# Kernel optimization log

Hardware: AMD Instinct MI355X
Metric: run time of the kernel (lower is better)

Reference implementation:

```python
import jax, jax.numpy as jnp
import numpy as np

N_NODES = 100000
N_EDGES = 800000
D = 64   # embedding_size
H = 4    # heads


def setup_inputs() -> dict:
    key = jax.random.key(0)
    k1, k2, k3, k4, k5 = jax.random.split(key, 5)
    xavier = float(np.sqrt(2.0 / (D + D)))  # xavier_uniform scale (approx, via normal)
    all_embeddings = jax.random.normal(k1, (N_NODES, D), dtype=jnp.float32)
    Wq = jax.random.normal(k2, (D, D), dtype=jnp.float32) * xavier
    Wk = jax.random.normal(k3, (D, D), dtype=jnp.float32) * xavier
    Wv = jax.random.normal(k4, (D, D), dtype=jnp.float32) * xavier
    edge_index = jax.random.randint(k5, (2, N_EDGES), 0, N_NODES, dtype=jnp.int32)
    return {"all_embeddings": all_embeddings, "Wq": Wq, "Wk": Wk, "Wv": Wv,
            "edge_index": edge_index}


def reference(all_embeddings, Wq, Wk, Wv, edge_index):
    rows, cols = edge_index[0], edge_index[1]
    n_nodes = all_embeddings.shape[0]
    e = rows.shape[0]
    dh = D // H

    row_emb = all_embeddings[rows]           # [E, D] gather
    col_emb = all_embeddings[cols]           # [E, D] gather

    q = (row_emb @ Wq).reshape(e, H, dh)     # [E, H, dh]
    k = (col_emb @ Wk).reshape(e, H, dh)
    v = (col_emb @ Wv).reshape(e, H, dh)

    att = jnp.einsum('ehd,ehd->eh', q, k)    # per-edge, per-head score
    att = jnp.clip(att, -10.0, 10.0)
    exp_att = jnp.exp(att)                   # [E, H]

    # segment softmax denominator over edges sharing the same destination row
    att_norm = jax.ops.segment_sum(exp_att, rows, num_segments=n_nodes)  # [N, H]
    att = exp_att / (att_norm[rows] + 1e-8)  # [E, H]

    out_e = (att[:, :, None] * v).reshape(e, D)  # [E, D] weighted values
    out = jax.ops.segment_sum(out_e, rows, num_segments=n_nodes)  # [N, D] scatter-add
    return out
```

## Files before the change

kernel.cpp:

```cpp
#include <hip/hip_runtime.h>
#include <math.h>

constexpr int D = 64;
constexpr int H = 4;
constexpr int EB = 8192;


typedef __attribute__((ext_vector_type(8))) short bf16x8;
typedef __attribute__((ext_vector_type(4))) float f32x4;

__device__ __forceinline__ unsigned short f32_to_bf16(float f) {
    const unsigned int u = __float_as_uint(f);
    return (unsigned short)((u + 0x7FFFu + ((u >> 16) & 1u)) >> 16);
}
__device__ __forceinline__ float bf16_to_f32(unsigned short h) {
    return __uint_as_float(((unsigned int)h) << 16);
}
__device__ __forceinline__ float bf16lo_f32(unsigned int w) {
    return __uint_as_float(w << 16);
}
__device__ __forceinline__ float bf16hi_f32(unsigned int w) {
    return __uint_as_float(w & 0xFFFF0000u);
}

__global__ __launch_bounds__(256) void prep_w_kernel(
    const float* __restrict__ Wq, const float* __restrict__ Wk,
    const float* __restrict__ Wv,
    unsigned short* __restrict__ WfH, unsigned short* __restrict__ WfL) {
    const float* W[3] = {Wq, Wk, Wv};
    for (int idx = blockIdx.x * 256 + threadIdx.x; idx < 3 * 4 * 2 * 64 * 8;
         idx += gridDim.x * 256) {
        const int j  = idx & 7;
        const int l  = (idx >> 3) & 63;
        const int ks = (idx >> 9) & 1;
        const int ct = (idx >> 10) & 3;
        const int mt = idx >> 12;
        const int krow = ks * 32 + (l >> 4) * 8 + j;
        const int col  = 4 * (l & 15) + ct;
        const float w  = W[mt][krow * 64 + col];
        const unsigned short h = f32_to_bf16(w);
        WfH[idx] = h;
        WfL[idx] = f32_to_bf16(w - bf16_to_f32(h));
    }
}

__global__ __launch_bounds__(256) void fused_qkv_hist_kernel(
    const float* __restrict__ emb,
    const unsigned short* __restrict__ WfH,
    const unsigned short* __restrict__ WfL,
    int N, float* __restrict__ Q, unsigned int* __restrict__ KVP,
    const int* __restrict__ rows, int* __restrict__ hist2d,
    int E, int NB, int HB) {
    __shared__ unsigned short sH[12288];
    __shared__ unsigned short sL[12288];
    __shared__ int h[512];
    const int tid = threadIdx.x;

    if ((int)blockIdx.x < HB) {
        const int blk = blockIdx.x;
        for (int b = tid; b < NB; b += 256) h[b] = 0;
        __syncthreads();
        const int e0 = blk * EB;
        const int e1 = min(E, e0 + EB);
        for (int i = e0 + tid; i < e1; i += 256)
            atomicAdd(&h[rows[i] >> 8], 1);
        __syncthreads();
        for (int b = tid; b < NB; b += 256) hist2d[blk * NB + b] = h[b];
        return;
    }

    const int bx = blockIdx.x - HB;
    {
        const uint4* gh = (const uint4*)WfH;
        const uint4* gl = (const uint4*)WfL;
        uint4* shh = (uint4*)sH;
        uint4* sll = (uint4*)sL;
        for (int k = tid; k < 1536; k += 256) {
            shh[k] = gh[k];
            sll[k] = gl[k];
        }
    }
    __syncthreads();

    const int wv = tid >> 6;
    const int l  = tid & 63;
    const int qd = l >> 4;
    const int m  = l & 15;

    for (int tile = 0; tile < 4; ++tile) {
        const int n0 = bx * 256 + tile * 64 + wv * 16;
        if (n0 >= N) break;

        bf16x8 aH[2], aL[2];
        {
            int node = n0 + m;
            if (node >= N) node = N - 1;
            const float4* ep = (const float4*)(emb + (size_t)node * 64);
#pragma unroll
            for (int ks = 0; ks < 2; ++ks) {
                const float4 a0 = ep[ks * 8 + qd * 2 + 0];
                const float4 a1 = ep[ks * 8 + qd * 2 + 1];
                const float f[8] = {a0.x, a0.y, a0.z, a0.w,
                                    a1.x, a1.y, a1.z, a1.w};
                bf16x8 fh, fl;
#pragma unroll
                for (int j = 0; j < 8; ++j) {
                    const unsigned short hh = f32_to_bf16(f[j]);
                    fh[j] = (short)hh;
                    fl[j] = (short)f32_to_bf16(f[j] - bf16_to_f32(hh));
                }
                aH[ks] = fh;
                aL[ks] = fl;
            }
        }

        f32x4 acc[3][4];
#pragma unroll
        for (int mt = 0; mt < 3; ++mt)
#pragma unroll
            for (int ct = 0; ct < 4; ++ct)
                acc[mt][ct] = (f32x4){0.f, 0.f, 0.f, 0.f};

#pragma unroll
        for (int mt = 0; mt < 3; ++mt) {
#pragma unroll
            for (int ct = 0; ct < 4; ++ct) {
#pragma unroll
                for (int ks = 0; ks < 2; ++ks) {
                    const int fi = (((mt * 4 + ct) * 2 + ks) * 64 + l) * 8;
                    bf16x8 bh = *(const bf16x8*)&sH[fi];
                    bf16x8 bl = *(const bf16x8*)&sL[fi];
                    acc[mt][ct] = __builtin_amdgcn_mfma_f32_16x16x32_bf16(
                        aH[ks], bh, acc[mt][ct], 0, 0, 0);
                    acc[mt][ct] = __builtin_amdgcn_mfma_f32_16x16x32_bf16(
                        aH[ks], bl, acc[mt][ct], 0, 0, 0);
                    acc[mt][ct] = __builtin_amdgcn_mfma_f32_16x16x32_bf16(
                        aL[ks], bh, acc[mt][ct], 0, 0, 0);
                }
            }
        }

#pragma unroll
        for (int r = 0; r < 4; ++r) {
            const int node = n0 + qd * 4 + r;
            if (node < N) {
                float4 oq;
                oq.x = acc[0][0][r]; oq.y = acc[0][1][r];
                oq.z = acc[0][2][r]; oq.w = acc[0][3][r];
                *(float4*)(Q + (size_t)node * 64 + 4 * m) = oq;

                uint4 kv;
                kv.x = (unsigned int)f32_to_bf16(acc[1][0][r]) |
                       ((unsigned int)f32_to_bf16(acc[1][1][r]) << 16);
                kv.y = (unsigned int)f32_to_bf16(acc[2][0][r]) |
                       ((unsigned int)f32_to_bf16(acc[2][1][r]) << 16);
                kv.z = (unsigned int)f32_to_bf16(acc[1][2][r]) |
                       ((unsigned int)f32_to_bf16(acc[1][3][r]) << 16);
                kv.w = (unsigned int)f32_to_bf16(acc[2][2][r]) |
                       ((unsigned int)f32_to_bf16(acc[2][3][r]) << 16);
                *(uint4*)(KVP + (size_t)node * 64 + 4 * m) = kv;
            }
        }
    }
}

__global__ __launch_bounds__(256) void scan2d_kernel(
    const int* __restrict__ hist2d, int* __restrict__ base2d,
    int* __restrict__ btot, int NBLK, int NB) {
    __shared__ int s[256];
    const int b   = blockIdx.x;
    const int tid = threadIdx.x;
    const int x = (tid < NBLK) ? hist2d[tid * NB + b] : 0;
    s[tid] = x;
    __syncthreads();
    for (int o = 1; o < 256; o <<= 1) {
        int v = 0;
        if (tid >= o) v = s[tid - o];
        __syncthreads();
        if (tid >= o) s[tid] += v;
        __syncthreads();
    }
    if (tid < NBLK) base2d[tid * NB + b] = s[tid] - x;
    if (tid == 255) btot[b] = s[255];
}

__global__ __launch_bounds__(256) void bscan_kernel(
    const int* __restrict__ btot, int* __restrict__ bbase, int NB) {
    __shared__ int s[256];
    __shared__ int carry;
    const int tid = threadIdx.x;
    if (tid == 0) carry = 0;
    __syncthreads();
    for (int base = 0; base < NB; base += 256) {
        const int i = base + tid;
        const int x = (i < NB) ? btot[i] : 0;
        s[tid] = x;
        __syncthreads();
        for (int o = 1; o < 256; o <<= 1) {
            int v = 0;
            if (tid >= o) v = s[tid - o];
            __syncthreads();
            if (tid >= o) s[tid] += v;
            __syncthreads();
        }
        if (i < NB) bbase[i] = carry + s[tid] - x;
        __syncthreads();
        if (tid == 255) carry += s[255];
        __syncthreads();
    }
}

__global__ __launch_bounds__(256) void scatter2d_kernel(
    const int* __restrict__ rows, const int* __restrict__ cols,
    const int* __restrict__ base2d, const int* __restrict__ bbase,
    unsigned int* __restrict__ tmp, int E, int NB) {
    __shared__ int lcur[512];
    const int tid = threadIdx.x;
    const int blk = blockIdx.x;
    for (int b = tid; b < NB; b += 256)
        lcur[b] = bbase[b] + base2d[blk * NB + b];
    __syncthreads();
    const int e0 = blk * EB;
    const int e1 = min(E, e0 + EB);
    for (int i = e0 + tid; i < e1; i += 256) {
        const int r = rows[i];
        const int c = cols[i];
        const int p = atomicAdd(&lcur[r >> 8], 1);
        tmp[p] = ((unsigned int)(r & 255) << 24) | (unsigned int)c;
    }
}

__global__ __launch_bounds__(256) void bucket_sort_kernel(
    const unsigned int* __restrict__ tmp, const int* __restrict__ bbase,
    const int* __restrict__ btot, int* __restrict__ off,
    int* __restrict__ sc, int N, int E, int NB) {
    __shared__ unsigned int ebuf[4096];
    __shared__ int sbuf[4096];
    __shared__ int lhist[256];
    __shared__ int s[256];
    __shared__ int lcur[256];
    const int b     = blockIdx.x;
    const int tid   = threadIdx.x;
    const int n0    = b * 256;
    const int gbase = bbase[b];
    const int cnt_b = btot[b];

    lhist[tid] = 0;
    __syncthreads();

    if (cnt_b <= 4096) {
        for (int i = tid; i < cnt_b; i += 256) {
            const unsigned int w = tmp[gbase + i];
            ebuf[i] = w;
            atomicAdd(&lhist[w >> 24], 1);
        }
        __syncthreads();
        const int x = lhist[tid];
        s[tid] = x;
        __syncthreads();
        for (int o = 1; o < 256; o <<= 1) {
            int v = 0;
            if (tid >= o) v = s[tid - o];
            __syncthreads();
            if (tid >= o) s[tid] += v;
            __syncthreads();
        }
        const int excl = s[tid] - x;
        const int node = n0 + tid;
        if (node < N) off[node] = gbase + excl;
        if (b == NB - 1 && tid == 0) off[N] = E;
        lcur[tid] = excl;
        __syncthreads();
        for (int i = tid; i < cnt_b; i += 256) {
            const unsigned int w = ebuf[i];
            const int p = atomicAdd(&lcur[w >> 24], 1);
            sbuf[p] = (int)(w & 0x00FFFFFFu);
        }
        __syncthreads();
        for (int i = tid; i < cnt_b; i += 256) sc[gbase + i] = sbuf[i];
    } else {
        for (int i = tid; i < cnt_b; i += 256)
            atomicAdd(&lhist[tmp[gbase + i] >> 24], 1);
        __syncthreads();
        const int x = lhist[tid];
        s[tid] = x;
        __syncthreads();
        for (int o = 1; o < 256; o <<= 1) {
            int v = 0;
            if (tid >= o) v = s[tid - o];
            __syncthreads();
            if (tid >= o) s[tid] += v;
            __syncthreads();
        }
        const int excl = s[tid] - x;
        const int node = n0 + tid;
        if (node < N) off[node] = gbase + excl;
        if (b == NB - 1 && tid == 0) off[N] = E;
        lcur[tid] = excl;
        __syncthreads();
        for (int i = tid; i < cnt_b; i += 256) {
            const unsigned int w = tmp[gbase + i];
            const int p = atomicAdd(&lcur[w >> 24], 1);
            sc[gbase + p] = (int)(w & 0x00FFFFFFu);
        }
    }
}

__device__ __forceinline__ void agg_step(const uint4 kv, const float4 q4,
                                         bool ok, float& aN, float& a0,
                                         float& a1, float& a2, float& a3) {
    float pp = q4.x * bf16lo_f32(kv.x);
    pp = fmaf(q4.y, bf16hi_f32(kv.x), pp);
    pp = fmaf(q4.z, bf16lo_f32(kv.z), pp);
    pp = fmaf(q4.w, bf16hi_f32(kv.z), pp);
    pp += __shfl_xor(pp, 1);
    pp += __shfl_xor(pp, 2);
    float e = __expf(fminf(fmaxf(pp, -10.f), 10.f));
    e = ok ? e : 0.f;
    aN += e;
    a0 = fmaf(e, bf16lo_f32(kv.y), a0);
    a1 = fmaf(e, bf16hi_f32(kv.y), a1);
    a2 = fmaf(e, bf16lo_f32(kv.w), a2);
    a3 = fmaf(e, bf16hi_f32(kv.w), a3);
}

__global__ __launch_bounds__(256) void aggregate_kernel(
    const int* __restrict__ off, const int* __restrict__ sc,
    const float* __restrict__ Q, const unsigned int* __restrict__ KVP,
    float* __restrict__ out, int N) {
    const int t = blockIdx.x * 256 + threadIdx.x;
    const int n = t >> 6;
    const int l = t & 63;
    if (n >= N) return;
    const int d  = l & 15;
    const int es = l >> 4;

    const int off0 = off[n];
    const int off1 = off[n + 1];
    const int deg  = off1 - off0;
    const float4 q4 = *(const float4*)(Q + (size_t)n * 64 + 4 * d);

    float aN = 0.f, a0 = 0.f, a1 = 0.f, a2 = 0.f, a3 = 0.f;

    for (int base = 0; base < deg; base += 64) {
        const int cnt = min(64, deg - base);
        int myc = 0;
        if (l < cnt) myc = sc[off0 + base + l];
        const int nst = (cnt + 3) >> 2;
        int si = 0;
        for (; si + 4 <= nst; si += 4) {
            const int e0 = si * 4 + es;
            const bool ok3 = e0 + 12 < cnt;
            const int c0 = __shfl(myc, e0);
            const int c1 = __shfl(myc, e0 + 4);
            const int c2 = __shfl(myc, e0 + 8);
            const int c3 = __shfl(myc, ok3 ? e0 + 12 : 0);
            const uint4 kv0 = *(const uint4*)(KVP + (size_t)c0 * 64 + 4 * d);
            const uint4 kv1 = *(const uint4*)(KVP + (size_t)c1 * 64 + 4 * d);
            const uint4 kv2 = *(const uint4*)(KVP + (size_t)c2 * 64 + 4 * d);
            const uint4 kv3 = *(const uint4*)(KVP + (size_t)c3 * 64 + 4 * d);
            agg_step(kv0, q4, true, aN, a0, a1, a2, a3);
            agg_step(kv1, q4, true, aN, a0, a1, a2, a3);
            agg_step(kv2, q4, true, aN, a0, a1, a2, a3);
            agg_step(kv3, q4, ok3, aN, a0, a1, a2, a3);
        }
        if (si + 2 <= nst) {
            const int e0 = si * 4 + es;
            const bool ok1 = e0 + 4 < cnt;
            const int c0 = __shfl(myc, e0);
            const int c1 = __shfl(myc, ok1 ? e0 + 4 : 0);
            const uint4 kv0 = *(const uint4*)(KVP + (size_t)c0 * 64 + 4 * d);
            const uint4 kv1 = *(const uint4*)(KVP + (size_t)c1 * 64 + 4 * d);
            agg_step(kv0, q4, true, aN, a0, a1, a2, a3);
            agg_step(kv1, q4, ok1, aN, a0, a1, a2, a3);
            si += 2;
        }
        if (si < nst) {
            const int e0 = si * 4 + es;
            const bool ok0 = e0 < cnt;
            const int c0 = __shfl(myc, ok0 ? e0 : 0);
            const uint4 kv0 = *(const uint4*)(KVP + (size_t)c0 * 64 + 4 * d);
            agg_step(kv0, q4, ok0, aN, a0, a1, a2, a3);
        }
    }

    aN += __shfl_xor(aN, 16);  aN += __shfl_xor(aN, 32);
    a0 += __shfl_xor(a0, 16);  a0 += __shfl_xor(a0, 32);
    a1 += __shfl_xor(a1, 16);  a1 += __shfl_xor(a1, 32);
    a2 += __shfl_xor(a2, 16);  a2 += __shfl_xor(a2, 32);
    a3 += __shfl_xor(a3, 16);  a3 += __shfl_xor(a3, 32);

    if (l < 16) {
        const float inv = 1.f / (aN + 1e-8f);
        float4 o;
        o.x = a0 * inv;
        o.y = a1 * inv;
        o.z = a2 * inv;
        o.w = a3 * inv;
        *(float4*)(out + (size_t)n * 64 + 4 * d) = o;
    }
}

extern "C" void kernel_launch(void* const* d_in, const int* in_sizes, int n_in,
                              void* d_out, int out_size, void* d_ws, size_t ws_size,
                              hipStream_t stream) {
    const float* emb = (const float*)d_in[0];
    const float* Wq  = (const float*)d_in[1];
    const float* Wk  = (const float*)d_in[2];
    const float* Wv  = (const float*)d_in[3];
    const int*   w32 = (const int*)d_in[4];

    const int N    = in_sizes[0] / D;
    const int E    = in_sizes[4] / 2;
    const int NB   = (N + 255) / 256;
    const int NBLK = (E + EB - 1) / EB;
    const int QB   = (N + 255) / 256;
    const size_t ND = (size_t)N * D;

    const int* rows = w32;
    const int* cols = w32 + E;

    unsigned short* WfH = (unsigned short*)d_ws;
    unsigned short* WfL = WfH + 12288;
    float*          Q   = (float*)(WfL + 12288);
    unsigned int*   KVP = (unsigned int*)(Q + ND);
    int*   off  = (int*)(KVP + ND);
    int*   sc   = off + N + 2;
    unsigned int* tmp = (unsigned int*)(sc + E);
    int*   hist2d = (int*)(tmp + E);
    int*   base2d = hist2d + NBLK * NB;
    int*   btot   = base2d + NBLK * NB;
    int*   bbase  = btot + NB;

    float* out = (float*)d_out;

    prep_w_kernel<<<48, 256, 0, stream>>>(Wq, Wk, Wv, WfH, WfL);

    fused_qkv_hist_kernel<<<NBLK + QB, 256, 0, stream>>>(
        emb, WfH, WfL, N, Q, KVP, rows, hist2d, E, NB, NBLK);

    scan2d_kernel<<<NB, 256, 0, stream>>>(hist2d, base2d, btot, NBLK, NB);
    bscan_kernel<<<1, 256, 0, stream>>>(btot, bbase, NB);
    scatter2d_kernel<<<NBLK, 256, 0, stream>>>(rows, cols, base2d, bbase,
                                               tmp, E, NB);
    bucket_sort_kernel<<<NB, 256, 0, stream>>>(tmp, bbase, btot, off, sc,
                                               N, E, NB);

    aggregate_kernel<<<((size_t)N * 64 + 255) / 256, 256, 0, stream>>>(
        off, sc, Q, KVP, out, N);
}
```

Baseline: 164.9 us.

## Pack per-node degree, offset and first neighbor ids into padded records

The bucket sort kernel now writes a 48-int record per node holding its degree, its CSR offset and up to 46 neighbor column ids. The aggregate kernel reads this record with one coalesced wave load instead of two dependent reads (the offsets, then the sorted column list). Only nodes with more than 46 neighbors fall back to reading the CSR list. The cost is about 19 MB of extra writes per call, and in the bucket sort each thread writes its own record serially, so the stores are strided and poorly coalesced.

```diff
diff --git a/kernel.cpp b/kernel.cpp
--- a/kernel.cpp
+++ b/kernel.cpp
@@ -4,6 +4,7 @@
 constexpr int D = 64;
 constexpr int H = 4;
 constexpr int EB = 8192;
+constexpr int PADC = 46;
 
 
 typedef __attribute__((ext_vector_type(8))) short bf16x8;
@@ -232,7 +233,7 @@
 
 __global__ __launch_bounds__(256) void bucket_sort_kernel(
     const unsigned int* __restrict__ tmp, const int* __restrict__ bbase,
-    const int* __restrict__ btot, int* __restrict__ off,
+    const int* __restrict__ btot, int* __restrict__ pvec,
     int* __restrict__ sc, int N, int E, int NB) {
     __shared__ unsigned int ebuf[4096];
     __shared__ int sbuf[4096];
@@ -266,9 +267,6 @@
             __syncthreads();
         }
         const int excl = s[tid] - x;
-        const int node = n0 + tid;
-        if (node < N) off[node] = gbase + excl;
-        if (b == NB - 1 && tid == 0) off[N] = E;
         lcur[tid] = excl;
         __syncthreads();
         for (int i = tid; i < cnt_b; i += 256) {
@@ -278,6 +276,14 @@
         }
         __syncthreads();
         for (int i = tid; i < cnt_b; i += 256) sc[gbase + i] = sbuf[i];
+        const int node = n0 + tid;
+        if (node < N) {
+            int* rec = pvec + (size_t)node * 48;
+            rec[0] = x;
+            rec[1] = gbase + excl;
+            const int m = min(x, PADC);
+            for (int j = 0; j < m; ++j) rec[2 + j] = sbuf[excl + j];
+        }
     } else {
         for (int i = tid; i < cnt_b; i += 256)
             atomicAdd(&lhist[tmp[gbase + i] >> 24], 1);
@@ -293,15 +299,21 @@
             __syncthreads();
         }
         const int excl = s[tid] - x;
-        const int node = n0 + tid;
-        if (node < N) off[node] = gbase + excl;
-        if (b == NB - 1 && tid == 0) off[N] = E;
         lcur[tid] = excl;
         __syncthreads();
         for (int i = tid; i < cnt_b; i += 256) {
             const unsigned int w = tmp[gbase + i];
             const int p = atomicAdd(&lcur[w >> 24], 1);
             sc[gbase + p] = (int)(w & 0x00FFFFFFu);
+        }
+        __syncthreads();
+        const int node = n0 + tid;
+        if (node < N) {
+            int* rec = pvec + (size_t)node * 48;
+            rec[0] = x;
+            rec[1] = gbase + excl;
+            const int m = min(x, PADC);
+            for (int j = 0; j < m; ++j) rec[2 + j] = sc[gbase + excl + j];
         }
     }
 }
@@ -325,7 +337,7 @@
 }
 
 __global__ __launch_bounds__(256) void aggregate_kernel(
-    const int* __restrict__ off, const int* __restrict__ sc,
+    const int* __restrict__ pvec, const int* __restrict__ sc,
     const float* __restrict__ Q, const unsigned int* __restrict__ KVP,
     float* __restrict__ out, int N) {
     const int t = blockIdx.x * 256 + threadIdx.x;
@@ -335,26 +347,24 @@
     const int d  = l & 15;
     const int es = l >> 4;
 
-    const int off0 = off[n];
-    const int off1 = off[n + 1];
-    const int deg  = off1 - off0;
+    int w = 0;
+    if (l < 48) w = pvec[(size_t)n * 48 + l];
     const float4 q4 = *(const float4*)(Q + (size_t)n * 64 + 4 * d);
+    const int deg = __shfl(w, 0);
 
     float aN = 0.f, a0 = 0.f, a1 = 0.f, a2 = 0.f, a3 = 0.f;
 
-    for (int base = 0; base < deg; base += 64) {
-        const int cnt = min(64, deg - base);
-        int myc = 0;
-        if (l < cnt) myc = sc[off0 + base + l];
-        const int nst = (cnt + 3) >> 2;
+    if (deg > 0) {
+        const int cnt0 = min(deg, PADC);
+        const int nst = (cnt0 + 3) >> 2;
         int si = 0;
         for (; si + 4 <= nst; si += 4) {
             const int e0 = si * 4 + es;
-            const bool ok3 = e0 + 12 < cnt;
-            const int c0 = __shfl(myc, e0);
-            const int c1 = __shfl(myc, e0 + 4);
-            const int c2 = __shfl(myc, e0 + 8);
-            const int c3 = __shfl(myc, ok3 ? e0 + 12 : 0);
+            const bool ok3 = e0 + 12 < cnt0;
+            const int c0 = __shfl(w, 2 + e0);
+            const int c1 = __shfl(w, 2 + e0 + 4);
+            const int c2 = __shfl(w, 2 + e0 + 8);
+            const int c3 = __shfl(w, ok3 ? 2 + e0 + 12 : 2);
             const uint4 kv0 = *(const uint4*)(KVP + (size_t)c0 * 64 + 4 * d);
             const uint4 kv1 = *(const uint4*)(KVP + (size_t)c1 * 64 + 4 * d);
             const uint4 kv2 = *(const uint4*)(KVP + (size_t)c2 * 64 + 4 * d);
@@ -366,9 +376,9 @@
         }
         if (si + 2 <= nst) {
             const int e0 = si * 4 + es;
-            const bool ok1 = e0 + 4 < cnt;
-            const int c0 = __shfl(myc, e0);
-            const int c1 = __shfl(myc, ok1 ? e0 + 4 : 0);
+            const bool ok1 = e0 + 4 < cnt0;
+            const int c0 = __shfl(w, 2 + e0);
+            const int c1 = __shfl(w, ok1 ? 2 + e0 + 4 : 2);
             const uint4 kv0 = *(const uint4*)(KVP + (size_t)c0 * 64 + 4 * d);
             const uint4 kv1 = *(const uint4*)(KVP + (size_t)c1 * 64 + 4 * d);
             agg_step(kv0, q4, true, aN, a0, a1, a2, a3);
@@ -377,10 +387,54 @@
         }
         if (si < nst) {
             const int e0 = si * 4 + es;
-            const bool ok0 = e0 < cnt;
-            const int c0 = __shfl(myc, ok0 ? e0 : 0);
+            const bool ok0 = e0 < cnt0;
+            const int c0 = __shfl(w, ok0 ? 2 + e0 : 2);
             const uint4 kv0 = *(const uint4*)(KVP + (size_t)c0 * 64 + 4 * d);
             agg_step(kv0, q4, ok0, aN, a0, a1, a2, a3);
+        }
+        if (deg > PADC) {
+            const int off0 = __shfl(w, 1);
+            for (int base = PADC; base < deg; base += 64) {
+                const int cnt = min(64, deg - base);
+                int myc = 0;
+                if (l < cnt) myc = sc[off0 + base + l];
+                const int nst2 = (cnt + 3) >> 2;
+                int sj = 0;
+                for (; sj + 4 <= nst2; sj += 4) {
+                    const int e0 = sj * 4 + es;
+                    const bool ok3 = e0 + 12 < cnt;
+                    const int c0 = __shfl(myc, e0);
+                    const int c1 = __shfl(myc, e0 + 4);
+                    const int c2 = __shfl(myc, e0 + 8);
+                    const int c3 = __shfl(myc, ok3 ? e0 + 12 : 0);
+                    const uint4 kv0 = *(const uint4*)(KVP + (size_t)c0 * 64 + 4 * d);
+                    const uint4 kv1 = *(const uint4*)(KVP + (size_t)c1 * 64 + 4 * d);
+                    const uint4 kv2 = *(const uint4*)(KVP + (size_t)c2 * 64 + 4 * d);
+                    const uint4 kv3 = *(const uint4*)(KVP + (size_t)c3 * 64 + 4 * d);
+                    agg_step(kv0, q4, true, aN, a0, a1, a2, a3);
+                    agg_step(kv1, q4, true, aN, a0, a1, a2, a3);
+                    agg_step(kv2, q4, true, aN, a0, a1, a2, a3);
+                    agg_step(kv3, q4, ok3, aN, a0, a1, a2, a3);
+                }
+                if (sj + 2 <= nst2) {
+                    const int e0 = sj * 4 + es;
+                    const bool ok1 = e0 + 4 < cnt;
+                    const int c0 = __shfl(myc, e0);
+                    const int c1 = __shfl(myc, ok1 ? e0 + 4 : 0);
+                    const uint4 kv0 = *(const uint4*)(KVP + (size_t)c0 * 64 + 4 * d);
+                    const uint4 kv1 = *(const uint4*)(KVP + (size_t)c1 * 64 + 4 * d);
+                    agg_step(kv0, q4, true, aN, a0, a1, a2, a3);
+                    agg_step(kv1, q4, ok1, aN, a0, a1, a2, a3);
+                    sj += 2;
+                }
+                if (sj < nst2) {
+                    const int e0 = sj * 4 + es;
+                    const bool ok0 = e0 < cnt;
+                    const int c0 = __shfl(myc, ok0 ? e0 : 0);
+                    const uint4 kv0 = *(const uint4*)(KVP + (size_t)c0 * 64 + 4 * d);
+                    agg_step(kv0, q4, ok0, aN, a0, a1, a2, a3);
+                }
+            }
         }
     }
 
@@ -424,8 +478,8 @@
     unsigned short* WfL = WfH + 12288;
     float*          Q   = (float*)(WfL + 12288);
     unsigned int*   KVP = (unsigned int*)(Q + ND);
-    int*   off  = (int*)(KVP + ND);
-    int*   sc   = off + N + 2;
+    int*   pvec = (int*)(KVP + ND);
+    int*   sc   = pvec + (size_t)N * 48;
     unsigned int* tmp = (unsigned int*)(sc + E);
     int*   hist2d = (int*)(tmp + E);
     int*   base2d = hist2d + NBLK * NB;
@@ -443,9 +497,9 @@
     bscan_kernel<<<1, 256, 0, stream>>>(btot, bbase, NB);
     scatter2d_kernel<<<NBLK, 256, 0, stream>>>(rows, cols, base2d, bbase,
                                                tmp, E, NB);
-    bucket_sort_kernel<<<NB, 256, 0, stream>>>(tmp, bbase, btot, off, sc,
+    bucket_sort_kernel<<<NB, 256, 0, stream>>>(tmp, bbase, btot, pvec, sc,
                                                N, E, NB);
 
     aggregate_kernel<<<((size_t)N * 64 + 255) / 256, 256, 0, stream>>>(
-        off, sc, Q, KVP, out, N);
-}
+        pvec, sc, Q, KVP, out, N);
+}
```

Result: no change. 165.2 us (+0.2%).

## Pack per-node degree, offset and inline neighbor list; process four nodes per wave

Applied to the files above, without the earlier changes.

The bucket sort now writes a 16-int record per node holding degree, offset and up to 14 inlined neighbor indices, replacing the separate offset array. The aggregate kernel assigns four nodes per wavefront, with 16 lanes per node. Each wavefront reads the four records in one coalesced load and gathers neighbor K/V rows directly from the inlined indices. Nodes with more than 14 neighbors fall back to a serial loop over the sorted neighbor array. This removes the dependent off/sc loads and the idle lanes that low-degree nodes left in the one-node-per-wave scheme, at the cost of an extra 64 bytes of record writes per node and lane divergence when degrees differ within a wave.

```diff
diff --git a/kernel.cpp b/kernel.cpp
--- a/kernel.cpp
+++ b/kernel.cpp
@@ -4,6 +4,7 @@
 constexpr int D = 64;
 constexpr int H = 4;
 constexpr int EB = 8192;
+constexpr int INL = 14;
 
 
 typedef __attribute__((ext_vector_type(8))) short bf16x8;
@@ -232,7 +233,7 @@
 
 __global__ __launch_bounds__(256) void bucket_sort_kernel(
     const unsigned int* __restrict__ tmp, const int* __restrict__ bbase,
-    const int* __restrict__ btot, int* __restrict__ off,
+    const int* __restrict__ btot, int* __restrict__ pvec,
     int* __restrict__ sc, int N, int E, int NB) {
     __shared__ unsigned int ebuf[4096];
     __shared__ int sbuf[4096];
@@ -266,9 +267,6 @@
             __syncthreads();
         }
         const int excl = s[tid] - x;
-        const int node = n0 + tid;
-        if (node < N) off[node] = gbase + excl;
-        if (b == NB - 1 && tid == 0) off[N] = E;
         lcur[tid] = excl;
         __syncthreads();
         for (int i = tid; i < cnt_b; i += 256) {
@@ -278,6 +276,14 @@
         }
         __syncthreads();
         for (int i = tid; i < cnt_b; i += 256) sc[gbase + i] = sbuf[i];
+        const int node = n0 + tid;
+        if (node < N) {
+            int* rec = pvec + (size_t)node * 16;
+            rec[0] = x;
+            rec[1] = gbase + excl;
+            const int m = min(x, INL);
+            for (int j = 0; j < m; ++j) rec[2 + j] = sbuf[excl + j];
+        }
     } else {
         for (int i = tid; i < cnt_b; i += 256)
             atomicAdd(&lhist[tmp[gbase + i] >> 24], 1);
@@ -293,15 +299,21 @@
             __syncthreads();
         }
         const int excl = s[tid] - x;
-        const int node = n0 + tid;
-        if (node < N) off[node] = gbase + excl;
-        if (b == NB - 1 && tid == 0) off[N] = E;
         lcur[tid] = excl;
         __syncthreads();
         for (int i = tid; i < cnt_b; i += 256) {
             const unsigned int w = tmp[gbase + i];
             const int p = atomicAdd(&lcur[w >> 24], 1);
             sc[gbase + p] = (int)(w & 0x00FFFFFFu);
+        }
+        __syncthreads();
+        const int node = n0 + tid;
+        if (node < N) {
+            int* rec = pvec + (size_t)node * 16;
+            rec[0] = x;
+            rec[1] = gbase + excl;
+            const int m = min(x, INL);
+            for (int j = 0; j < m; ++j) rec[2 + j] = sc[gbase + excl + j];
         }
     }
 }
@@ -325,79 +337,86 @@
 }
 
 __global__ __launch_bounds__(256) void aggregate_kernel(
-    const int* __restrict__ off, const int* __restrict__ sc,
+    const int* __restrict__ pv16, const int* __restrict__ sc,
     const float* __restrict__ Q, const unsigned int* __restrict__ KVP,
     float* __restrict__ out, int N) {
-    const int t = blockIdx.x * 256 + threadIdx.x;
-    const int n = t >> 6;
-    const int l = t & 63;
-    if (n >= N) return;
+    const int wid = (blockIdx.x * 256 + threadIdx.x) >> 6;
+    const int l   = threadIdx.x & 63;
+    const int nbase = wid * 4;
+    if (nbase >= N) return;
+    const int ns = l >> 4;
     const int d  = l & 15;
-    const int es = l >> 4;
-
-    const int off0 = off[n];
-    const int off1 = off[n + 1];
-    const int deg  = off1 - off0;
-    const float4 q4 = *(const float4*)(Q + (size_t)n * 64 + 4 * d);
+    const int node  = nbase + ns;
+    const int nodec = min(node, N - 1);
+
+    const int w = pv16[(size_t)nbase * 16 + l];
+    const int w0 = __shfl(w, ns * 16);
+    const int deg  = (node < N) ? w0 : 0;
+    const int off0 = __shfl(w, ns * 16 + 1);
+    const float4 q4 = *(const float4*)(Q + (size_t)nodec * 64 + 4 * d);
 
     float aN = 0.f, a0 = 0.f, a1 = 0.f, a2 = 0.f, a3 = 0.f;
 
-    for (int base = 0; base < deg; base += 64) {
-        const int cnt = min(64, deg - base);
-        int myc = 0;
-        if (l < cnt) myc = sc[off0 + base + l];
-        const int nst = (cnt + 3) >> 2;
-        int si = 0;
-        for (; si + 4 <= nst; si += 4) {
-            const int e0 = si * 4 + es;
-            const bool ok3 = e0 + 12 < cnt;
-            const int c0 = __shfl(myc, e0);
-            const int c1 = __shfl(myc, e0 + 4);
-            const int c2 = __shfl(myc, e0 + 8);
-            const int c3 = __shfl(myc, ok3 ? e0 + 12 : 0);
-            const uint4 kv0 = *(const uint4*)(KVP + (size_t)c0 * 64 + 4 * d);
-            const uint4 kv1 = *(const uint4*)(KVP + (size_t)c1 * 64 + 4 * d);
-            const uint4 kv2 = *(const uint4*)(KVP + (size_t)c2 * 64 + 4 * d);
-            const uint4 kv3 = *(const uint4*)(KVP + (size_t)c3 * 64 + 4 * d);
-            agg_step(kv0, q4, true, aN, a0, a1, a2, a3);
-            agg_step(kv1, q4, true, aN, a0, a1, a2, a3);
-            agg_step(kv2, q4, true, aN, a0, a1, a2, a3);
-            agg_step(kv3, q4, ok3, aN, a0, a1, a2, a3);
-        }
-        if (si + 2 <= nst) {
-            const int e0 = si * 4 + es;
-            const bool ok1 = e0 + 4 < cnt;
-            const int c0 = __shfl(myc, e0);
-            const int c1 = __shfl(myc, ok1 ? e0 + 4 : 0);
-            const uint4 kv0 = *(const uint4*)(KVP + (size_t)c0 * 64 + 4 * d);
-            const uint4 kv1 = *(const uint4*)(KVP + (size_t)c1 * 64 + 4 * d);
-            agg_step(kv0, q4, true, aN, a0, a1, a2, a3);
-            agg_step(kv1, q4, ok1, aN, a0, a1, a2, a3);
-            si += 2;
-        }
-        if (si < nst) {
-            const int e0 = si * 4 + es;
-            const bool ok0 = e0 < cnt;
-            const int c0 = __shfl(myc, ok0 ? e0 : 0);
-            const uint4 kv0 = *(const uint4*)(KVP + (size_t)c0 * 64 + 4 * d);
-            agg_step(kv0, q4, ok0, aN, a0, a1, a2, a3);
-        }
-    }
-
-    aN += __shfl_xor(aN, 16);  aN += __shfl_xor(aN, 32);
-    a0 += __shfl_xor(a0, 16);  a0 += __shfl_xor(a0, 32);
-    a1 += __shfl_xor(a1, 16);  a1 += __shfl_xor(a1, 32);
-    a2 += __shfl_xor(a2, 16);  a2 += __shfl_xor(a2, 32);
-    a3 += __shfl_xor(a3, 16);  a3 += __shfl_xor(a3, 32);
-
-    if (l < 16) {
+    const int cin = min(deg, INL);
+    int mc = cin;
+    mc = max(mc, __shfl_xor(mc, 16));
+    mc = max(mc, __shfl_xor(mc, 32));
+
+    int i = 0;
+    for (; i + 4 <= mc; i += 4) {
+        const bool o0 = i + 0 < cin, o1 = i + 1 < cin,
+                   o2 = i + 2 < cin, o3 = i + 3 < cin;
+        int c0 = __shfl(w, ns * 16 + 2 + i + 0); c0 = o0 ? c0 : 0;
+        int c1 = __shfl(w, ns * 16 + 2 + i + 1); c1 = o1 ? c1 : 0;
+        int c2 = __shfl(w, ns * 16 + 2 + i + 2); c2 = o2 ? c2 : 0;
+        int c3 = __shfl(w, ns * 16 + 2 + i + 3); c3 = o3 ? c3 : 0;
+        const uint4 kv0 = *(const uint4*)(KVP + (size_t)c0 * 64 + 4 * d);
+        const uint4 kv1 = *(const uint4*)(KVP + (size_t)c1 * 64 + 4 * d);
+        const uint4 kv2 = *(const uint4*)(KVP + (size_t)c2 * 64 + 4 * d);
+        const uint4 kv3 = *(const uint4*)(KVP + (size_t)c3 * 64 + 4 * d);
+        agg_step(kv0, q4, o0, aN, a0, a1, a2, a3);
+        agg_step(kv1, q4, o1, aN, a0, a1, a2, a3);
+        agg_step(kv2, q4, o2, aN, a0, a1, a2, a3);
+        agg_step(kv3, q4, o3, aN, a0, a1, a2, a3);
+    }
+    if (i + 2 <= mc) {
+        const bool o0 = i + 0 < cin, o1 = i + 1 < cin;
+        int c0 = __shfl(w, ns * 16 + 2 + i + 0); c0 = o0 ? c0 : 0;
+        int c1 = __shfl(w, ns * 16 + 2 + i + 1); c1 = o1 ? c1 : 0;
+        const uint4 kv0 = *(const uint4*)(KVP + (size_t)c0 * 64 + 4 * d);
+        const uint4 kv1 = *(const uint4*)(KVP + (size_t)c1 * 64 + 4 * d);
+        agg_step(kv0, q4, o0, aN, a0, a1, a2, a3);
+        agg_step(kv1, q4, o1, aN, a0, a1, a2, a3);
+        i += 2;
+    }
+    if (i < mc) {
+        const bool o0 = i < cin;
+        int c0 = __shfl(w, ns * 16 + 2 + i); c0 = o0 ? c0 : 0;
+        const uint4 kv0 = *(const uint4*)(KVP + (size_t)c0 * 64 + 4 * d);
+        agg_step(kv0, q4, o0, aN, a0, a1, a2, a3);
+    }
+
+    if (__any(deg > INL)) {
+        const int cnt2 = max(deg - INL, 0);
+        int mt = cnt2;
+        mt = max(mt, __shfl_xor(mt, 16));
+        mt = max(mt, __shfl_xor(mt, 32));
+        for (int i2 = 0; i2 < mt; ++i2) {
+            const bool ok = i2 < cnt2;
+            const int c = ok ? sc[off0 + INL + i2] : 0;
+            const uint4 kv = *(const uint4*)(KVP + (size_t)c * 64 + 4 * d);
+            agg_step(kv, q4, ok, aN, a0, a1, a2, a3);
+        }
+    }
+
+    if (node < N) {
         const float inv = 1.f / (aN + 1e-8f);
         float4 o;
         o.x = a0 * inv;
         o.y = a1 * inv;
         o.z = a2 * inv;
         o.w = a3 * inv;
-        *(float4*)(out + (size_t)n * 64 + 4 * d) = o;
+        *(float4*)(out + (size_t)node * 64 + 4 * d) = o;
     }
 }
 
@@ -415,6 +434,7 @@
     const int NB   = (N + 255) / 256;
     const int NBLK = (E + EB - 1) / EB;
     const int QB   = (N + 255) / 256;
+    const int NW   = (N + 3) / 4;
     const size_t ND = (size_t)N * D;
 
     const int* rows = w32;
@@ -424,8 +444,8 @@
     unsigned short* WfL = WfH + 12288;
     float*          Q   = (float*)(WfL + 12288);
     unsigned int*   KVP = (unsigned int*)(Q + ND);
-    int*   off  = (int*)(KVP + ND);
-    int*   sc   = off + N + 2;
+    int*   pvec = (int*)(KVP + ND);
+    int*   sc   = pvec + (size_t)(NW * 4) * 16;
     unsigned int* tmp = (unsigned int*)(sc + E);
     int*   hist2d = (int*)(tmp + E);
     int*   base2d = hist2d + NBLK * NB;
@@ -443,9 +463,9 @@
     bscan_kernel<<<1, 256, 0, stream>>>(btot, bbase, NB);
     scatter2d_kernel<<<NBLK, 256, 0, stream>>>(rows, cols, base2d, bbase,
                                                tmp, E, NB);
-    bucket_sort_kernel<<<NB, 256, 0, stream>>>(tmp, bbase, btot, off, sc,
+    bucket_sort_kernel<<<NB, 256, 0, stream>>>(tmp, bbase, btot, pvec, sc,
                                                N, E, NB);
 
-    aggregate_kernel<<<((size_t)N * 64 + 255) / 256, 256, 0, stream>>>(
-        off, sc, Q, KVP, out, N);
-}
+    aggregate_kernel<<<((size_t)NW * 64 + 255) / 256, 256, 0, stream>>>(
+        pvec, sc, Q, KVP, out, N);
+}
```

Measured after the change: 168.7 us. +2.3%, slower.
